# Kernel tuning notes

Hardware: AMD Instinct MI355X
Metric: run time of the kernel (lower is better)

## Reference

```python
import jax, jax.numpy as jnp
import numpy as np

DK, DL, HID = 128, 128, 128  # per init_kwargs: mlp_list=[256,128,128]


def setup_inputs() -> dict:
    key = jax.random.key(0)
    k1, k2, k3, k4, k5 = jax.random.split(key, 5)
    B, K, L = 2, 128, 4096
    inputA = jax.random.normal(k1, (B, K, DK), dtype=jnp.float32)
    inputB = jax.random.normal(k2, (B, L, DL), dtype=jnp.float32)
    # MLP layer 0: Linear(256 -> 128), kaiming-uniform-ish init
    lim1 = 1.0 / np.sqrt(DK + DL)
    W1 = jax.random.uniform(k3, (DK + DL, HID), jnp.float32, -lim1, lim1)
    b1 = jax.random.uniform(k4, (HID,), jnp.float32, -lim1, lim1)
    # scoring Linear(128 -> 1, bias=False)
    lim2 = 1.0 / np.sqrt(HID)
    w2 = jax.random.uniform(k5, (HID,), jnp.float32, -lim2, lim2)
    return {"inputA": inputA, "inputB": inputB, "W1": W1, "b1": b1,
            "w2": w2, "nA": K, "nB": L}


def reference(inputA, inputB, W1, b1, w2, nA, nB):
    # Original: tC = cat([repeat(A), repeat(B)], -1); mlp(tC); linear; softmax(L).
    # Fused-equivalent math: split W1 rows between the A-part and B-part of the
    # concat, so the first Linear is two small matmuls + broadcast add.
    hA = jnp.einsum('bkd,dh->bkh', inputA, W1[:DK])        # (B, K, H)
    hB = jnp.einsum('bld,dh->blh', inputB, W1[DK:])        # (B, L, H)
    h = jax.nn.relu(hA[:, :, None, :] + hB[:, None, :, :] + b1)  # (B, K, L, H)
    scores = jnp.einsum('bklh,h->bkl', h, w2)              # (B, K, L)
    return jax.nn.softmax(scores, axis=2)
```

## Files before the change

kernel.cpp:

```cpp
#include <hip/hip_runtime.h>
#include <hip/hip_fp16.h>
#include <math.h>

constexpr int BB = 2;
constexpr int KK = 128;
constexpr int LL = 4096;
constexpr int DD = 128;
constexpr int HH = 128;

__device__ __forceinline__ float4 ld4(const float* p) {
    return *reinterpret_cast<const float4*>(p);
}

__device__ __forceinline__ __half2 hmax2(__half2 a, __half2 b) {
    unsigned ua = __builtin_bit_cast(unsigned, a);
    unsigned ub = __builtin_bit_cast(unsigned, b);
    unsigned ud;
    asm("v_pk_max_f16 %0, %1, %2" : "=v"(ud) : "v"(ua), "v"(ub));
    return __builtin_bit_cast(__half2, ud);
}

__device__ __forceinline__ uint32_t duph(float x) {
    __half h = __float2half(x);
    unsigned short us = __builtin_bit_cast(unsigned short, h);
    return (uint32_t)us * 0x10001u;
}

__global__ __launch_bounds__(256) void k1_gemm(
    const float* __restrict__ inA, const float* __restrict__ inB,
    const float* __restrict__ W1, const float* __restrict__ b1,
    const float* __restrict__ w2,
    uint32_t* __restrict__ u_dup, uint32_t* __restrict__ w2_dup,
    __half* __restrict__ vT)
{
    __shared__ __align__(16) float sIn[32 * 128];
    __shared__ float sT[128 * 33];

    const int row0 = blockIdx.x * 32;
    const bool isA = (row0 < BB * KK);
    const float* src = isA ? (inA + (size_t)row0 * DD)
                           : (inB + (size_t)(row0 - BB * KK) * DD);
    const float* w   = W1 + (isA ? 0 : DD * HH);

    const int tid = threadIdx.x;

    #pragma unroll
    for (int j = 0; j < 4; ++j) {
        const int idx = tid + 256 * j;
        reinterpret_cast<float4*>(sIn)[idx] =
            reinterpret_cast<const float4*>(src)[idx];
    }
    __syncthreads();

    const int tx = tid & 31;
    const int ty = tid >> 5;

    float accx[4], accy[4], accz[4], accw[4];
    #pragma unroll
    for (int r = 0; r < 4; ++r) { accx[r] = accy[r] = accz[r] = accw[r] = 0.f; }

    for (int d0 = 0; d0 < DD; d0 += 4) {
        float4 w4[4];
        #pragma unroll
        for (int dd = 0; dd < 4; ++dd)
            w4[dd] = ld4(&w[(size_t)(d0 + dd) * HH + tx * 4]);
        float a[4][4];
        #pragma unroll
        for (int r = 0; r < 4; ++r) {
            float4 a4 = ld4(&sIn[(ty * 4 + r) * 128 + d0]);
            a[r][0] = a4.x; a[r][1] = a4.y; a[r][2] = a4.z; a[r][3] = a4.w;
        }
        #pragma unroll
        for (int dd = 0; dd < 4; ++dd) {
            const float4 wv = w4[dd];
            #pragma unroll
            for (int r = 0; r < 4; ++r) {
                const float av = a[r][dd];
                accx[r] = fmaf(av, wv.x, accx[r]);
                accy[r] = fmaf(av, wv.y, accy[r]);
                accz[r] = fmaf(av, wv.z, accz[r]);
                accw[r] = fmaf(av, wv.w, accw[r]);
            }
        }
    }

    if (isA) {
        const float4 bb = ld4(&b1[tx * 4]);
        #pragma unroll
        for (int r = 0; r < 4; ++r) {
            uint4 o;
            o.x = duph(accx[r] + bb.x);
            o.y = duph(accy[r] + bb.y);
            o.z = duph(accz[r] + bb.z);
            o.w = duph(accw[r] + bb.w);
            *reinterpret_cast<uint4*>(&u_dup[(size_t)(row0 + ty * 4 + r) * HH + tx * 4]) = o;
        }
        if (blockIdx.x == 0 && tid < HH) w2_dup[tid] = duph(w2[tid]);
    } else {
        #pragma unroll
        for (int r = 0; r < 4; ++r) {
            const int l = ty * 4 + r;
            sT[(tx * 4 + 0) * 33 + l] = accx[r];
            sT[(tx * 4 + 1) * 33 + l] = accy[r];
            sT[(tx * 4 + 2) * 33 + l] = accz[r];
            sT[(tx * 4 + 3) * 33 + l] = accw[r];
        }
        __syncthreads();
        const int h    = tid >> 1;
        const int half = tid & 1;
        const int rowB = row0 - BB * KK;
        const int bsel = rowB >> 12;
        const int l0   = (rowB & 4095) + half * 16;
        uint32_t o[8];
        #pragma unroll
        for (int i = 0; i < 8; ++i) {
            const float lo = sT[h * 33 + half * 16 + 2 * i];
            const float hi = sT[h * 33 + half * 16 + 2 * i + 1];
            o[i] = __builtin_bit_cast(uint32_t, __floats2half2_rn(lo, hi));
        }
        uint32_t* dst = reinterpret_cast<uint32_t*>(vT) +
                        ((size_t)(bsel * HH + h) * LL + l0) / 2;
        uint4 s0; s0.x = o[0]; s0.y = o[1]; s0.z = o[2]; s0.w = o[3];
        uint4 s1; s1.x = o[4]; s1.y = o[5]; s1.z = o[6]; s1.w = o[7];
        *reinterpret_cast<uint4*>(dst)     = s0;
        *reinterpret_cast<uint4*>(dst + 4) = s1;
    }
}

__global__ __launch_bounds__(256) void k2_score(
    const uint32_t* __restrict__ u_dup, const uint32_t* __restrict__ w2_dup,
    const __half* __restrict__ vT, float* __restrict__ out)
{
    int bi = blockIdx.x;
    const int kt = bi & 31;  bi >>= 5;
    const int lt = bi & 7;   bi >>= 3;
    const int b  = bi;
    const int tid = threadIdx.x;

    const int lp = lt * 256 + tid;
    const uint32_t* vp = reinterpret_cast<const uint32_t*>(vT)
                         + (size_t)b * HH * (LL / 2) + lp;
    const uint32_t* up = u_dup + (size_t)(b * KK + kt * 4) * HH;

    float2 facc[4];
    #pragma unroll
    for (int k = 0; k < 4; ++k) { facc[k].x = 0.f; facc[k].y = 0.f; }

    const __half2 hz = __float2half2_rn(0.f);

    for (int g = 0; g < 8; ++g) {
        __half2 acc[4];
        #pragma unroll
        for (int k = 0; k < 4; ++k) acc[k] = hz;

        #pragma unroll
        for (int c = 0; c < 2; ++c) {
            const int h0 = g * 16 + c * 8;
            uint32_t v[8];
            #pragma unroll
            for (int j = 0; j < 8; ++j)
                v[j] = vp[(size_t)(h0 + j) * (LL / 2)];
            #pragma unroll
            for (int k = 0; k < 4; ++k) {
                #pragma unroll
                for (int j = 0; j < 8; ++j) {
                    const __half2 uu = __builtin_bit_cast(__half2, up[k * HH + h0 + j]);
                    const __half2 ww = __builtin_bit_cast(__half2, w2_dup[h0 + j]);
                    __half2 t = __hadd2(__builtin_bit_cast(__half2, v[j]), uu);
                    acc[k] = __hfma2(hmax2(t, hz), ww, acc[k]);
                }
            }
        }
        #pragma unroll
        for (int k = 0; k < 4; ++k) {
            const float2 f = __half22float2(acc[k]);
            facc[k].x += f.x; facc[k].y += f.y;
        }
    }

    #pragma unroll
    for (int k = 0; k < 4; ++k)
        *reinterpret_cast<float2*>(
            &out[(size_t)(b * KK + kt * 4 + k) * LL + 2 * lp]) = facc[k];
}

__global__ __launch_bounds__(256) void k3_softmax(float* __restrict__ out)
{
    __shared__ float redm[4];
    __shared__ float reds[4];

    const int row = blockIdx.x;
    float* p = out + (size_t)row * LL;
    const int tid = threadIdx.x;

    float4 x[4];
    #pragma unroll
    for (int j = 0; j < 4; ++j)
        x[j] = reinterpret_cast<const float4*>(p)[tid + 256 * j];

    float m = x[0].x;
    #pragma unroll
    for (int j = 0; j < 4; ++j)
        m = fmaxf(m, fmaxf(fmaxf(x[j].x, x[j].y), fmaxf(x[j].z, x[j].w)));
    #pragma unroll
    for (int off = 32; off > 0; off >>= 1)
        m = fmaxf(m, __shfl_xor(m, off, 64));

    const int lane = tid & 63, wv = tid >> 6;
    if (lane == 0) redm[wv] = m;
    __syncthreads();
    m = fmaxf(fmaxf(redm[0], redm[1]), fmaxf(redm[2], redm[3]));

    float s = 0.f;
    #pragma unroll
    for (int j = 0; j < 4; ++j) {
        x[j].x = expf(x[j].x - m); s += x[j].x;
        x[j].y = expf(x[j].y - m); s += x[j].y;
        x[j].z = expf(x[j].z - m); s += x[j].z;
        x[j].w = expf(x[j].w - m); s += x[j].w;
    }
    #pragma unroll
    for (int off = 32; off > 0; off >>= 1)
        s += __shfl_xor(s, off, 64);
    if (lane == 0) reds[wv] = s;
    __syncthreads();
    s = (reds[0] + reds[1]) + (reds[2] + reds[3]);

    const float inv = 1.0f / s;
    #pragma unroll
    for (int j = 0; j < 4; ++j) {
        x[j].x *= inv; x[j].y *= inv; x[j].z *= inv; x[j].w *= inv;
        reinterpret_cast<float4*>(p)[tid + 256 * j] = x[j];
    }
}

extern "C" void kernel_launch(void* const* d_in, const int* in_sizes, int n_in,
                              void* d_out, int out_size, void* d_ws, size_t ws_size,
                              hipStream_t stream)
{
    const float* inA = (const float*)d_in[0];
    const float* inB = (const float*)d_in[1];
    const float* W1  = (const float*)d_in[2];
    const float* b1  = (const float*)d_in[3];
    const float* w2  = (const float*)d_in[4];
    float* out = (float*)d_out;

    uint32_t* u_dup  = (uint32_t*)d_ws;
    uint32_t* w2_dup = (uint32_t*)((char*)d_ws + 128 * 1024);
    __half*   vT     = (__half*)((char*)d_ws + 128 * 1024 + 512);

    hipLaunchKernelGGL(k1_gemm, dim3(264), dim3(256), 0, stream,
                       inA, inB, W1, b1, w2, u_dup, w2_dup, vT);
    hipLaunchKernelGGL(k2_score, dim3(512), dim3(256), 0, stream,
                       u_dup, w2_dup, vT, out);
    hipLaunchKernelGGL(k3_softmax, dim3(BB * KK), dim3(256), 0, stream, out);
}
```

Before: 33.01 us.

## Fuse score computation with row softmax in a single 1024-thread kernel

Replaces the separate score and softmax kernels with one kernel where each block computes a full score row for one k and performs the softmax in registers with block-wide reductions. This removes the global write and reread of the score matrix and one kernel launch. In exchange, the vT data is no longer reused across several k rows per load, so L2 read traffic for vT grows, and parallelism drops to one large block per row.

New measurement: 32.78 us. No clear change (-0.7%).

```diff
diff --git a/kernel.cpp b/kernel.cpp
--- a/kernel.cpp
+++ b/kernel.cpp
@@ -93,7 +93,8 @@
             o.y = duph(accy[r] + bb.y);
             o.z = duph(accz[r] + bb.z);
             o.w = duph(accw[r] + bb.w);
-            *reinterpret_cast<uint4*>(&u_dup[(size_t)(row0 + ty * 4 + r) * HH + tx * 4]) = o;
+            *reinterpret_cast<uint4*>(
+                &u_dup[(size_t)(row0 + ty * 4 + r) * HH + tx * 4]) = o;
         }
         if (blockIdx.x == 0 && tid < HH) w2_dup[tid] = duph(w2[tid]);
     } else {
@@ -127,111 +128,111 @@
     }
 }
 
-__global__ __launch_bounds__(256) void k2_score(
+__global__ __launch_bounds__(1024) void k2_fused(
     const uint32_t* __restrict__ u_dup, const uint32_t* __restrict__ w2_dup,
     const __half* __restrict__ vT, float* __restrict__ out)
 {
-    int bi = blockIdx.x;
-    const int kt = bi & 31;  bi >>= 5;
-    const int lt = bi & 7;   bi >>= 3;
-    const int b  = bi;
+    __shared__ __align__(16) uint32_t sU[HH];
+    __shared__ __align__(16) uint32_t sW[HH];
+    __shared__ float redm[16];
+    __shared__ float reds[16];
+
+    const int row = blockIdx.x;
+    const int b   = row >> 7;
     const int tid = threadIdx.x;
 
-    const int lp = lt * 256 + tid;
-    const uint32_t* vp = reinterpret_cast<const uint32_t*>(vT)
-                         + (size_t)b * HH * (LL / 2) + lp;
-    const uint32_t* up = u_dup + (size_t)(b * KK + kt * 4) * HH;
-
-    float2 facc[4];
-    #pragma unroll
-    for (int k = 0; k < 4; ++k) { facc[k].x = 0.f; facc[k].y = 0.f; }
+    if (tid < HH) sU[tid] = u_dup[(size_t)row * HH + tid];
+    else if (tid < 2 * HH) sW[tid - HH] = w2_dup[tid - HH];
+    __syncthreads();
+
+    const uint32_t* vpb = reinterpret_cast<const uint32_t*>(vT)
+                          + (size_t)b * HH * (LL / 2);
 
     const __half2 hz = __float2half2_rn(0.f);
 
+    float2 facc[2];
+    facc[0].x = 0.f; facc[0].y = 0.f;
+    facc[1].x = 0.f; facc[1].y = 0.f;
+
     for (int g = 0; g < 8; ++g) {
-        __half2 acc[4];
-        #pragma unroll
-        for (int k = 0; k < 4; ++k) acc[k] = hz;
-
-        #pragma unroll
-        for (int c = 0; c < 2; ++c) {
-            const int h0 = g * 16 + c * 8;
-            uint32_t v[8];
+        const int h0 = g * 16;
+        uint4 uc[4], wc[4];
+        #pragma unroll
+        for (int q = 0; q < 4; ++q) {
+            uc[q] = *reinterpret_cast<const uint4*>(&sU[h0 + q * 4]);
+            wc[q] = *reinterpret_cast<const uint4*>(&sW[h0 + q * 4]);
+        }
+        #pragma unroll
+        for (int p = 0; p < 2; ++p) {
+            const int lp = tid + p * 1024;
+            uint32_t v[16];
             #pragma unroll
-            for (int j = 0; j < 8; ++j)
-                v[j] = vp[(size_t)(h0 + j) * (LL / 2)];
+            for (int j = 0; j < 16; ++j)
+                v[j] = vpb[(size_t)(h0 + j) * (LL / 2) + lp];
+
+            __half2 acc = hz;
             #pragma unroll
-            for (int k = 0; k < 4; ++k) {
+            for (int q = 0; q < 4; ++q) {
+                const uint32_t* uq = reinterpret_cast<const uint32_t*>(&uc[q]);
+                const uint32_t* wq = reinterpret_cast<const uint32_t*>(&wc[q]);
                 #pragma unroll
-                for (int j = 0; j < 8; ++j) {
-                    const __half2 uu = __builtin_bit_cast(__half2, up[k * HH + h0 + j]);
-                    const __half2 ww = __builtin_bit_cast(__half2, w2_dup[h0 + j]);
-                    __half2 t = __hadd2(__builtin_bit_cast(__half2, v[j]), uu);
-                    acc[k] = __hfma2(hmax2(t, hz), ww, acc[k]);
+                for (int j = 0; j < 4; ++j) {
+                    const __half2 uu = __builtin_bit_cast(__half2, uq[j]);
+                    const __half2 ww = __builtin_bit_cast(__half2, wq[j]);
+                    const __half2 vv = __builtin_bit_cast(__half2, v[q * 4 + j]);
+                    __half2 t = __hadd2(vv, uu);
+                    acc = __hfma2(hmax2(t, hz), ww, acc);
                 }
             }
-        }
-        #pragma unroll
-        for (int k = 0; k < 4; ++k) {
-            const float2 f = __half22float2(acc[k]);
-            facc[k].x += f.x; facc[k].y += f.y;
-        }
-    }
-
-    #pragma unroll
-    for (int k = 0; k < 4; ++k)
-        *reinterpret_cast<float2*>(
-            &out[(size_t)(b * KK + kt * 4 + k) * LL + 2 * lp]) = facc[k];
-}
-
-__global__ __launch_bounds__(256) void k3_softmax(float* __restrict__ out)
-{
-    __shared__ float redm[4];
-    __shared__ float reds[4];
-
-    const int row = blockIdx.x;
-    float* p = out + (size_t)row * LL;
-    const int tid = threadIdx.x;
-
-    float4 x[4];
-    #pragma unroll
-    for (int j = 0; j < 4; ++j)
-        x[j] = reinterpret_cast<const float4*>(p)[tid + 256 * j];
-
-    float m = x[0].x;
-    #pragma unroll
-    for (int j = 0; j < 4; ++j)
-        m = fmaxf(m, fmaxf(fmaxf(x[j].x, x[j].y), fmaxf(x[j].z, x[j].w)));
+            const float2 f = __half22float2(acc);
+            facc[p].x += f.x; facc[p].y += f.y;
+        }
+    }
+
+    float m = fmaxf(fmaxf(facc[0].x, facc[0].y), fmaxf(facc[1].x, facc[1].y));
     #pragma unroll
     for (int off = 32; off > 0; off >>= 1)
         m = fmaxf(m, __shfl_xor(m, off, 64));
-
     const int lane = tid & 63, wv = tid >> 6;
     if (lane == 0) redm[wv] = m;
     __syncthreads();
-    m = fmaxf(fmaxf(redm[0], redm[1]), fmaxf(redm[2], redm[3]));
-
-    float s = 0.f;
-    #pragma unroll
-    for (int j = 0; j < 4; ++j) {
-        x[j].x = expf(x[j].x - m); s += x[j].x;
-        x[j].y = expf(x[j].y - m); s += x[j].y;
-        x[j].z = expf(x[j].z - m); s += x[j].z;
-        x[j].w = expf(x[j].w - m); s += x[j].w;
-    }
+    if (tid < 16) {
+        float mm = redm[tid];
+        #pragma unroll
+        for (int off = 8; off > 0; off >>= 1)
+            mm = fmaxf(mm, __shfl_xor(mm, off, 64));
+        redm[tid] = mm;
+    }
+    __syncthreads();
+    m = redm[0];
+
+    facc[0].x = expf(facc[0].x - m);
+    facc[0].y = expf(facc[0].y - m);
+    facc[1].x = expf(facc[1].x - m);
+    facc[1].y = expf(facc[1].y - m);
+    float s = (facc[0].x + facc[0].y) + (facc[1].x + facc[1].y);
     #pragma unroll
     for (int off = 32; off > 0; off >>= 1)
         s += __shfl_xor(s, off, 64);
     if (lane == 0) reds[wv] = s;
     __syncthreads();
-    s = (reds[0] + reds[1]) + (reds[2] + reds[3]);
+    if (tid < 16) {
+        float ss = reds[tid];
+        #pragma unroll
+        for (int off = 8; off > 0; off >>= 1)
+            ss += __shfl_xor(ss, off, 64);
+        reds[tid] = ss;
+    }
+    __syncthreads();
+    s = reds[0];
 
     const float inv = 1.0f / s;
-    #pragma unroll
-    for (int j = 0; j < 4; ++j) {
-        x[j].x *= inv; x[j].y *= inv; x[j].z *= inv; x[j].w *= inv;
-        reinterpret_cast<float4*>(p)[tid + 256 * j] = x[j];
-    }
+    float2 o0, o1;
+    o0.x = facc[0].x * inv; o0.y = facc[0].y * inv;
+    o1.x = facc[1].x * inv; o1.y = facc[1].y * inv;
+    float* po = out + (size_t)row * LL;
+    *reinterpret_cast<float2*>(&po[2 * tid])          = o0;
+    *reinterpret_cast<float2*>(&po[2 * (tid + 1024)]) = o1;
 }
 
 extern "C" void kernel_launch(void* const* d_in, const int* in_sizes, int n_in,
@@ -251,7 +252,6 @@
 
     hipLaunchKernelGGL(k1_gemm, dim3(264), dim3(256), 0, stream,
                        inA, inB, W1, b1, w2, u_dup, w2_dup, vT);
-    hipLaunchKernelGGL(k2_score, dim3(512), dim3(256), 0, stream,
+    hipLaunchKernelGGL(k2_fused, dim3(BB * KK), dim3(1024), 0, stream,
                        u_dup, w2_dup, vT, out);
-    hipLaunchKernelGGL(k3_softmax, dim3(BB * KK), dim3(256), 0, stream, out);
-}
+}
```
